# Optimization experiments

Measured on AMD Instinct MI355X. Metric: run time of the kernel, lower is better.

The kernel has to match this reference:

```python
import jax, jax.numpy as jnp
import numpy as np

EPS = 1e-5
BIG = np.int32(2 ** 30)      # sentinel larger than any voxel label
L_MAX = 1024                  # fixed upper bound on number of components (jit-friendly)


def _offsets(conn):
    # 3D neighborhood offsets with at most `conn` nonzero coordinates (skimage connectivity)
    offs = []
    for dz in (-1, 0, 1):
        for dy in (-1, 0, 1):
            for dx in (-1, 0, 1):
                nz = (dz != 0) + (dy != 0) + (dx != 0)
                if 0 < nz <= conn:
                    offs.append((dz, dy, dx))
    return offs


def _ccl_26(fg):
    """Connected-component labeling, 26-connectivity (skimage.label connectivity=3).
    Iterative min-label propagation (3x3x3 min-pool) + pointer jumping.
    Returns int32 labels: 0 = background, each component gets min(flat_index)+1."""
    shape = fg.shape
    n = fg.size
    init = jnp.where(fg, jnp.arange(1, n + 1, dtype=jnp.int32).reshape(shape), 0)

    def step(labels):
        cand = jnp.where(fg, labels, BIG)
        pooled = jax.lax.reduce_window(cand, BIG, jax.lax.min, (3, 3, 3), (1, 1, 1), 'SAME')
        new = jnp.where(fg, jnp.minimum(labels, pooled), 0)
        flat = new.ravel()
        for _ in range(2):  # pointer jumping / path compression (labels are flat_index+1)
            parent = flat[jnp.maximum(flat - 1, 0)]
            flat = jnp.where(flat > 0, parent, 0)
        return flat.reshape(shape)

    def cond(c):
        old, new = c
        return jnp.any(old != new)

    def body(c):
        _, cur = c
        return cur, step(cur)

    _, final = jax.lax.while_loop(cond, body, (init, step(init)))
    return final


def _inner_boundary_18(fg):
    """skimage find_boundaries(mode='inner', connectivity=2) on 3D binary mask:
    foreground voxel with any background voxel in its 18-neighborhood
    (fg & ~erosion(fg), reflect border handling)."""
    D, H, W = fg.shape
    p = jnp.pad(fg, 1, mode='reflect')
    eroded = fg
    for dz, dy, dx in _offsets(2):
        eroded = eroded & p[1 + dz:1 + dz + D, 1 + dy:1 + dy + H, 1 + dx:1 + dx + W]
    return fg & ~eroded


def _compactness(y_pred):
    fg = y_pred > 0.5
    labels = _ccl_26(fg)                       # [D,H,W] int32
    boundary = _inner_boundary_18(fg)          # [D,H,W] bool

    # compact per-component ids (sorted unique labels, padded with BIG to stay sorted)
    uniq = jnp.unique(labels, size=L_MAX, fill_value=BIG)
    ids = jnp.searchsorted(uniq, labels).astype(jnp.int32)

    area = jax.ops.segment_sum(fg.astype(jnp.float32).ravel(), ids.ravel(), num_segments=L_MAX)
    perim = jax.ops.segment_sum(boundary.astype(jnp.float32).ravel(), ids.ravel(), num_segments=L_MAX)

    valid = (uniq > 0) & (uniq < BIG)
    # sum over z of 4*pi*area_z / (perim_3d^2 + eps) == 4*pi*total_area / (perim^2 + eps),
    # then averaged over depth D (as in the original per-label /= shape[0]).
    per_label = jnp.where(valid, 4.0 * jnp.pi * area / (perim ** 2 + EPS), 0.0)
    return jnp.sum(per_label) / y_pred.shape[0]


def setup_inputs() -> dict:
    key = jax.random.key(0)
    y_pred = jax.random.uniform(key, (64, 256, 256), dtype=jnp.float32)
    return {"y_pred": y_pred}


def reference(y_pred) -> jnp.ndarray:
    comp = _compactness(y_pred)
    return 1.0 / (comp + EPS)
```

## Files before the change

### kernel.cpp

```cpp
#include <hip/hip_runtime.h>

#define DD 64
#define HH 256
#define WW 256
#define NN (DD*HH*WW)
#define GHS 2048
#define NCOPY 16
#define PHS 131072
#define NSEG (NN/32)

#define TZ 8
#define TY 32
#define TX 32
#define TVOX (TZ*TY*TX)

#define CA 458752
#define CB 114688
#define CFACE (CA + 4*CB)

__device__ __forceinline__ int ufind(int* P, int x){
  int p = P[x];
  while (p != x){
    int gp = P[p];
    if (gp != p) P[x] = gp;
    x = gp;
    p = P[x];
  }
  return x;
}

__device__ __forceinline__ int ufind_ro(const int* P, int x){
  int p = P[x];
  while (p != x){ x = p; p = P[x]; }
  return x;
}

__device__ __forceinline__ void uunion(int* P, int a, int b){
  while (true){
    a = ufind(P, a);
    b = ufind(P, b);
    if (a == b) return;
    if (a < b){ int t = a; a = b; b = t; }
    int old = atomicMin(&P[a], b);
    if (old == a) return;
    a = old;
  }
}

__device__ __forceinline__ int run_start(unsigned m, int x){
  unsigned zb = (~m) & ((x == 0) ? 0u : ((1u << x) - 1u));
  return (zb == 0) ? 0 : (32 - __builtin_clz(zb));
}

__device__ __forceinline__ int refl(int v, int L){ return v < 0 ? 1 : (v >= L ? L - 2 : v); }

__global__ __launch_bounds__(1024) void k_local(const float* __restrict__ in,
                                                int* __restrict__ parent,
                                                unsigned* __restrict__ fgbits,
                                                int* __restrict__ hkey,
                                                int* __restrict__ harea,
                                                int* __restrict__ hper,
                                                unsigned long long* __restrict__ ph){
  __shared__ int sl[TVOX];
  __shared__ unsigned srow[256];
  __shared__ int q[4096];
  __shared__ int qn;
  const int t = threadIdx.x;
  const int lane = t & 63;
  const int b = blockIdx.x;
  const int z0 = (b >> 6) * TZ;
  const int y0 = ((b >> 3) & 7) * TY;
  const int x0 = (b & 7) * TX;

  if (b < (NCOPY * GHS) / 1024){ int j = b * 1024 + t; hkey[j] = -1; harea[j] = 0; hper[j] = 0; }
  { int j = b * 1024 + t; if (j < PHS) ph[j] = ~0ULL; }
  if (t == 0) qn = 0;

  const int row = t >> 2;
  const int xb  = (t & 3) * 8;
  const int lz  = row >> 5, ly = row & 31;
  const int gi0 = ((z0 + lz) << 16) | ((y0 + ly) << 8) | (x0 + xb);

  float4 f0 = *(const float4*)(in + gi0);
  float4 f1 = *(const float4*)(in + gi0 + 4);
  int by = (f0.x > 0.5f)        | ((f0.y > 0.5f) << 1) |
           ((f0.z > 0.5f) << 2) | ((f0.w > 0.5f) << 3) |
           ((f1.x > 0.5f) << 4) | ((f1.y > 0.5f) << 5) |
           ((f1.z > 0.5f) << 6) | ((f1.w > 0.5f) << 7);
  int v1 = by | (__shfl_xor(by, 1) << 8);
  int v2 = v1 | (__shfl_xor(v1, 2) << 16);
  if ((t & 3) == 0){
    srow[row] = (unsigned)v2;
    fgbits[((z0 + lz) << 11) | ((y0 + ly) << 3) | (x0 >> 5)] = (unsigned)v2;
  }
  __syncthreads();

  const unsigned m = srow[row];
  const unsigned starts = m & ~(m << 1);
  const unsigned sm = starts & (0xFFu << xb);

  {
    int cnt = __popc(sm);
    int pre = cnt;
    #pragma unroll
    for (int d = 1; d < 64; d <<= 1){
      int v = __shfl_up(pre, d);
      if (lane >= d) pre += v;
    }
    int tot = __shfl(pre, 63);
    int bw = 0;
    if (lane == 63) bw = atomicAdd(&qn, tot);
    bw = __shfl(bw, 63);
    int pos = bw + pre - cnt;
    unsigned w = sm;
    while (w){
      int s = __builtin_ctz(w); w &= w - 1;
      int v = (row << 5) | s;
      sl[v] = v;
      q[pos++] = v;
    }
  }
  __syncthreads();
  const int NQ = qn;

  const int rel[4][2] = {{-1,-1},{-1,0},{-1,1},{0,-1}};
  for (int it = t; it < NQ; it += 1024){
    int v = q[it];
    int vrow = v >> 5, x = v & 31;
    unsigned mr = srow[vrow];
    unsigned zs = (~mr) >> x;
    int len = zs ? __builtin_ctz(zs) : (32 - x);
    int end = x + len - 1;
    unsigned long long wmask = ((1ull << (end + 2)) - 1) &
                               ~((x == 0) ? 0ull : ((1ull << (x - 1)) - 1));
    int vlz = vrow >> 5, vly = vrow & 31;
    #pragma unroll
    for (int r = 0; r < 4; r++){
      int zz = vlz + rel[r][0], yy = vly + rel[r][1];
      if (zz < 0 || yy < 0 || yy >= TY) continue;
      int nrow = (zz << 5) | yy;
      unsigned mN = srow[nrow];
      unsigned wm = mN & (unsigned)wmask;
      while (wm){
        int bb = __builtin_ctz(wm);
        int ns = run_start(mN, bb);
        uunion(sl, v, (nrow << 5) | ns);
        unsigned t2 = (~mN) >> bb;
        int l2 = t2 ? __builtin_ctz(t2) : (32 - bb);
        unsigned long long clr = (bb + l2 >= 32) ? 0xffffffffull : ((1ull << (bb + l2)) - 1);
        wm &= ~(unsigned)clr;
      }
    }
  }
  __syncthreads();

  for (int it = t; it < NQ; it += 1024){
    int v = q[it];
    sl[v] = ufind_ro(sl, v);
  }
  __syncthreads();

  int lab[8];
  int cur = -1;
  #pragma unroll
  for (int k = 0; k < 8; k++){
    int x = xb + k;
    if (!((m >> x) & 1)){ lab[k] = -1; cur = -1; continue; }
    if (cur < 0){
      int rs = (k == 0) ? run_start(m, x) : x;
      int r = sl[(row << 5) | rs];
      cur = ((z0 + (r >> 10)) << 16) | ((y0 + ((r >> 5) & 31)) << 8) | (x0 + (r & 31));
    }
    lab[k] = cur;
  }
  *(int4*)(parent + gi0)     = make_int4(lab[0], lab[1], lab[2], lab[3]);
  *(int4*)(parent + gi0 + 4) = make_int4(lab[4], lab[5], lab[6], lab[7]);
}

__device__ __forceinline__ void phash_union(unsigned long long* H, unsigned long long key,
                                            int* parent){
  unsigned h = (unsigned)((key * 0x9E3779B97F4A7C15ull) >> 47);
  while (true){
    unsigned long long old = atomicCAS(&H[h], ~0ULL, key);
    if (old == ~0ULL){ uunion(parent, (int)(key >> 32), (int)(key & 0xffffffffu)); return; }
    if (old == key) return;
    h = (h + 1) & (PHS - 1);
  }
}

__global__ __launch_bounds__(256) void k_pairs(int* __restrict__ parent,
                                               const unsigned* __restrict__ fgbits,
                                               unsigned long long* __restrict__ ph){
  __shared__ unsigned long long pk[256];
  const int t = threadIdx.x;
  pk[t] = ~0ULL;
  __syncthreads();

  const int nb = (int)gridDim.x;
  const int bsw = (blockIdx.x & 7) * (nb >> 3) + (blockIdx.x >> 3);
  const int id = bsw * 256 + t;
  int z, y, x, ot;
  if (id < CA){ ot = 0; z = ((id >> 16) + 1) << 3; y = (id >> 8) & 255; x = id & 255; }
  else {
    int q = id - CA;
    int f = q >> 14;
    int r = q & 16383;
    int g = f / 7, mm = f % 7;
    if      (g == 0){ ot = 1; y = (mm + 1) << 5;  z = r >> 8; x = r & 255; }
    else if (g == 1){ ot = 2; y = (mm << 5) + 31; z = r >> 8; x = r & 255; }
    else if (g == 2){ ot = 3; x = (mm + 1) << 5;  z = r >> 8; y = r & 255; }
    else            { ot = 4; x = (mm << 5) + 31; z = r >> 8; y = r & 255; }
  }
  const int s = x >> 5, xl = x & 31;
  const unsigned wself = fgbits[(z << 11) | (y << 3) | s];
  if ((wself >> xl) & 1){
    const int a = parent[(z << 16) | (y << 8) | x];
    unsigned long long lastkey = ~0ULL;

    auto do_pair = [&](int zz, int yy, int xc){
      int bl = parent[(zz << 16) | (yy << 8) | xc];
      int hi = a > bl ? a : bl, lo = a > bl ? bl : a;
      unsigned long long key = ((unsigned long long)(unsigned)hi << 32) | (unsigned)lo;
      if (key == lastkey) return;
      lastkey = key;
      unsigned h = (unsigned)((key * 0x9E3779B97F4A7C15ull) >> 56);
      for (int probe = 0; probe < 256; probe++){
        unsigned long long old = atomicCAS(&pk[h], ~0ULL, key);
        if (old == ~0ULL || old == key) return;
        h = (h + 1) & 255;
      }
      phash_union(ph, key, parent);
    };

    auto do_row = [&](int zz, int yy){
      if (zz < 0 || yy < 0 || yy >= HH) return;
      unsigned mN = fgbits[(zz << 11) | (yy << 3) | s];
      if ((mN >> xl) & 1){ do_pair(zz, yy, x); return; }
      bool l = (xl > 0) ? ((mN >> (xl - 1)) & 1)
                        : (x > 0 && ((fgbits[(zz << 11) | (yy << 3) | (s - 1)] >> 31) & 1));
      bool r = (xl < 31) ? ((mN >> (xl + 1)) & 1)
                         : (x < WW - 1 && (fgbits[(zz << 11) | (yy << 3) | (s + 1)] & 1));
      if (l) do_pair(zz, yy, x - 1);
      if (r) do_pair(zz, yy, x + 1);
    };

    auto do_bit = [&](int zz, int yy, int xc){
      if (zz < 0 || yy < 0 || yy >= HH) return;
      unsigned mN = fgbits[(zz << 11) | (yy << 3) | (xc >> 5)];
      if ((mN >> (xc & 31)) & 1) do_pair(zz, yy, xc);
    };

    switch (ot){
      case 0: do_row(z-1, y-1); do_row(z-1, y); do_row(z-1, y+1); break;
      case 1: do_row(z-1, y-1); do_row(z, y-1); break;
      case 2: do_row(z-1, y+1); break;
      case 3: do_bit(z-1, y-1, x-1); do_bit(z-1, y, x-1); do_bit(z-1, y+1, x-1);
              do_bit(z,   y-1, x-1); do_bit(z,   y, x-1); break;
      case 4: do_bit(z-1, y-1, x+1); do_bit(z-1, y, x+1); do_bit(z-1, y+1, x+1);
              do_bit(z,   y-1, x+1); break;
    }
  }
  __syncthreads();
  if (pk[t] != ~0ULL) phash_union(ph, pk[t], parent);
}

__device__ __forceinline__ void ghash_add(int* hkey, int* harea, int* hper,
                                          int key, int a, int p){
  unsigned h = ((unsigned)key * 2654435761u) >> 21;
  while (true){
    int old = atomicCAS(&hkey[h], -1, key);
    if (old == -1 || old == key){
      atomicAdd(&harea[h], a);
      if (p) atomicAdd(&hper[h], p);
      return;
    }
    h = (h + 1) & (GHS - 1);
  }
}

__global__ __launch_bounds__(1024) void k_stats(const int* __restrict__ parent,
                                                const unsigned* __restrict__ fgbits,
                                                int* __restrict__ hkey,
                                                int* __restrict__ harea,
                                                int* __restrict__ hper){
  __shared__ unsigned sfg[144];
  __shared__ unsigned sbnd[32];
  __shared__ int dk[256], da[256], dp[256];
  const int t = threadIdx.x;
  const int b = blockIdx.x;
  const int z = b >> 6;
  const int y0 = (b & 63) * 4;
  const int c = (b & (NCOPY - 1)) * GHS;

  if (t < 256){ dk[t] = -1; da[t] = 0; dp[t] = 0; }
  if (t < 144){
    int p = t / 48, q = (t / 8) % 6, s = t & 7;
    int zz = refl(z + p - 1, DD), yy = refl(y0 + q - 1, HH);
    sfg[t] = fgbits[(zz << 11) | (yy << 3) | s];
  }
  __syncthreads();

  if (t < 32){
    int ry = t >> 3, s = t & 7;
    auto W  = [&](int p, int q){ return sfg[p * 48 + q * 8 + s]; };
    auto WL = [&](int p, int q){
      unsigned w = W(p, q);
      unsigned c2 = (s > 0) ? ((sfg[p * 48 + q * 8 + s - 1] >> 31) & 1u) : ((w >> 1) & 1u);
      return (w << 1) | c2;
    };
    auto WR = [&](int p, int q){
      unsigned w = W(p, q);
      unsigned c2 = (s < 7) ? ((sfg[p * 48 + q * 8 + s + 1] & 1u) << 31) : ((w & 0x40000000u) << 1);
      return (w >> 1) | c2;
    };
    int qm = ry, qc = ry + 1, qp = ry + 2;
    unsigned own = W(1, qc);
    unsigned e = W(0, qm) & W(0, qp) & W(2, qm) & W(2, qp);
    e &= W(0, qc) & WL(0, qc) & WR(0, qc);
    e &= W(2, qc) & WL(2, qc) & WR(2, qc);
    e &= W(1, qm) & WL(1, qm) & WR(1, qm);
    e &= W(1, qp) & WL(1, qp) & WR(1, qp);
    e &= WL(1, qc) & WR(1, qc);
    sbnd[t] = own & ~e;
  }
  __syncthreads();

  const int i = b * 1024 + t;
  int lab = parent[i];
  int bnd = (lab >= 0) ? (int)((sbnd[t >> 5] >> (t & 31)) & 1) : 0;

  const int lane = t & 63;
  unsigned long long fgm = __ballot(lab >= 0);
  unsigned long long bm  = __ballot(bnd != 0);
  unsigned long long act = fgm;
  while (act){
    int leader = (int)__ffsll(act) - 1;
    int llab = __shfl(lab, leader);
    unsigned long long match = __ballot(lab == llab) & fgm;
    if (lane == leader){
      int a = (int)__popcll(match);
      int p = (int)__popcll(match & bm);
      unsigned h = ((unsigned)llab * 2654435761u) >> 24;
      bool done = false;
      for (int probe = 0; probe < 256; probe++){
        int old = atomicCAS(&dk[h], -1, llab);
        if (old == -1 || old == llab){
          atomicAdd(&da[h], a);
          if (p) atomicAdd(&dp[h], p);
          done = true; break;
        }
        h = (h + 1) & 255;
      }
      if (!done){
        int l2 = llab, pr = parent[l2];
        while (pr != l2){ l2 = pr; pr = parent[l2]; }
        ghash_add(hkey + c, harea + c, hper + c, l2, a, p);
      }
    }
    act &= ~match;
  }
  __syncthreads();
  if (t < 256 && dk[t] >= 0){
    int l2 = dk[t];
    int pr = parent[l2];
    while (pr != l2){ l2 = pr; pr = parent[l2]; }
    ghash_add(hkey + c, harea + c, hper + c, l2, da[t], dp[t]);
  }
}

__global__ __launch_bounds__(256) void k_merge(int* __restrict__ hkey,
                                               int* __restrict__ harea,
                                               int* __restrict__ hper){
  const int j = GHS + blockIdx.x * 256 + threadIdx.x;
  int key = hkey[j];
  if (key >= 0) ghash_add(hkey, harea, hper, key, harea[j], hper[j]);
}

__global__ __launch_bounds__(256) void k_fin(const int* __restrict__ hkey,
                                             const int* __restrict__ harea,
                                             const int* __restrict__ hper,
                                             float* __restrict__ out){
  __shared__ float ssum[256];
  const int t = threadIdx.x;
  float s = 0.0f;
  for (int j = t; j < GHS; j += 256){
    if (hkey[j] >= 0){
      float a = (float)harea[j];
      float p = (float)hper[j];
      s += 12.566370614359172f * a / (p * p + 1e-5f);
    }
  }
  ssum[t] = s;
  __syncthreads();
  for (int w = 128; w > 0; w >>= 1){
    if (t < w) ssum[t] += ssum[t + w];
    __syncthreads();
  }
  if (t == 0){
    float comp = ssum[0] / 64.0f;
    out[0] = 1.0f / (comp + 1e-5f);
  }
}

extern "C" void kernel_launch(void* const* d_in, const int* in_sizes, int n_in,
                              void* d_out, int out_size, void* d_ws, size_t ws_size,
                              hipStream_t stream){
  const float* y = (const float*)d_in[0];
  char* w = (char*)d_ws;
  int* parent            = (int*)w;                    w += (size_t)NN * 4;
  unsigned long long* ph = (unsigned long long*)w;     w += (size_t)PHS * 8;
  int* hkey              = (int*)w;                    w += (size_t)NCOPY * GHS * 4;
  int* harea             = (int*)w;                    w += (size_t)NCOPY * GHS * 4;
  int* hper              = (int*)w;                    w += (size_t)NCOPY * GHS * 4;
  unsigned* fgbits       = (unsigned*)w;               w += (size_t)NSEG * 4;
  float* out = (float*)d_out;

  hipLaunchKernelGGL(k_local, dim3(512),       dim3(1024), 0, stream, y, parent, fgbits, hkey, harea, hper, ph);
  hipLaunchKernelGGL(k_pairs, dim3(CFACE/256), dim3(256),  0, stream, parent, fgbits, ph);
  hipLaunchKernelGGL(k_stats, dim3(NN/1024),   dim3(1024), 0, stream, parent, fgbits, hkey, harea, hper);
  hipLaunchKernelGGL(k_merge, dim3((NCOPY-1)*GHS/256), dim3(256), 0, stream, hkey, harea, hper);
  hipLaunchKernelGGL(k_fin,   dim3(1),         dim3(256),  0, stream, hkey, harea, hper, out);
}
```

Before: 158.1 us.

## Shrink k_stats to one row per block and compute boundaries via wave shuffles

k_stats now runs 256-thread blocks that each cover a single (z,y) row, instead of 1024-thread blocks covering four rows. Each wave loads the 3x3 neighbouring bitmask words into registers and builds the 18-neighbour inner boundary with __shfl, replacing the shared-memory staging, the serial 32-thread boundary phase and a __syncthreads. This spreads the boundary work across all waves and shortens the per-block critical path. The cost is four times as many blocks, each flushing its local hash to the global tables, which adds global atomic traffic and contention on a few hot component keys.

```diff
diff --git a/kernel.cpp b/kernel.cpp
--- a/kernel.cpp
+++ b/kernel.cpp
@@ -278,58 +278,60 @@
   }
 }
 
-__global__ __launch_bounds__(1024) void k_stats(const int* __restrict__ parent,
-                                                const unsigned* __restrict__ fgbits,
-                                                int* __restrict__ hkey,
-                                                int* __restrict__ harea,
-                                                int* __restrict__ hper){
-  __shared__ unsigned sfg[144];
-  __shared__ unsigned sbnd[32];
+__global__ __launch_bounds__(256) void k_stats(const int* __restrict__ parent,
+                                               const unsigned* __restrict__ fgbits,
+                                               int* __restrict__ hkey,
+                                               int* __restrict__ harea,
+                                               int* __restrict__ hper){
   __shared__ int dk[256], da[256], dp[256];
   const int t = threadIdx.x;
   const int b = blockIdx.x;
-  const int z = b >> 6;
-  const int y0 = (b & 63) * 4;
+  const int z = b >> 8, y = b & 255;
+  const int lane = t & 63;
+  const int wv = t >> 6;
   const int c = (b & (NCOPY - 1)) * GHS;
 
-  if (t < 256){ dk[t] = -1; da[t] = 0; dp[t] = 0; }
-  if (t < 144){
-    int p = t / 48, q = (t / 8) % 6, s = t & 7;
-    int zz = refl(z + p - 1, DD), yy = refl(y0 + q - 1, HH);
-    sfg[t] = fgbits[(zz << 11) | (yy << 3) | s];
-  }
-  __syncthreads();
-
-  if (t < 32){
-    int ry = t >> 3, s = t & 7;
-    auto W  = [&](int p, int q){ return sfg[p * 48 + q * 8 + s]; };
-    auto WL = [&](int p, int q){
-      unsigned w = W(p, q);
-      unsigned c2 = (s > 0) ? ((sfg[p * 48 + q * 8 + s - 1] >> 31) & 1u) : ((w >> 1) & 1u);
-      return (w << 1) | c2;
-    };
-    auto WR = [&](int p, int q){
-      unsigned w = W(p, q);
-      unsigned c2 = (s < 7) ? ((sfg[p * 48 + q * 8 + s + 1] & 1u) << 31) : ((w & 0x40000000u) << 1);
-      return (w >> 1) | c2;
-    };
-    int qm = ry, qc = ry + 1, qp = ry + 2;
-    unsigned own = W(1, qc);
-    unsigned e = W(0, qm) & W(0, qp) & W(2, qm) & W(2, qp);
-    e &= W(0, qc) & WL(0, qc) & WR(0, qc);
-    e &= W(2, qc) & WL(2, qc) & WR(2, qc);
-    e &= W(1, qm) & WL(1, qm) & WR(1, qm);
-    e &= W(1, qp) & WL(1, qp) & WR(1, qp);
-    e &= WL(1, qc) & WR(1, qc);
-    sbnd[t] = own & ~e;
-  }
-  __syncthreads();
-
-  const int i = b * 1024 + t;
+  dk[t] = -1; da[t] = 0; dp[t] = 0;
+  __syncthreads();
+
+  unsigned wl = 0;
+  if (lane < 36){
+    int p = lane / 12, q = (lane / 4) % 3, d = lane & 3;
+    int ss = wv * 2 - 1 + d;
+    if (ss >= 0 && ss < 8){
+      int zz = refl(z + p - 1, DD), yy = refl(y + q - 1, HH);
+      wl = fgbits[(zz << 11) | (yy << 3) | ss];
+    }
+  }
+
+  const int j  = lane >> 5;
+  const int s  = wv * 2 + j;
+  const int xl = lane & 31;
+  auto SW = [&](int p, int q, int dd){ return (unsigned)__shfl((int)wl, p * 12 + q * 4 + j + 1 + dd, 64); };
+  auto W  = [&](int p, int q){ return SW(p, q, 0); };
+  auto WLf = [&](int p, int q){
+    unsigned w = W(p, q);
+    unsigned cc = (s > 0) ? ((SW(p, q, -1) >> 31) & 1u) : ((w >> 1) & 1u);
+    return (w << 1) | cc;
+  };
+  auto WRf = [&](int p, int q){
+    unsigned w = W(p, q);
+    unsigned cc = (s < 7) ? ((SW(p, q, +1) & 1u) << 31) : ((w & 0x40000000u) << 1);
+    return (w >> 1) | cc;
+  };
+  unsigned own = W(1, 1);
+  unsigned e = W(0, 0) & W(0, 2) & W(2, 0) & W(2, 2);
+  e &= W(0, 1) & WLf(0, 1) & WRf(0, 1);
+  e &= W(2, 1) & WLf(2, 1) & WRf(2, 1);
+  e &= W(1, 0) & WLf(1, 0) & WRf(1, 0);
+  e &= W(1, 2) & WLf(1, 2) & WRf(1, 2);
+  e &= WLf(1, 1) & WRf(1, 1);
+  const unsigned bndw = own & ~e;
+
+  const int i = b * 256 + t;
   int lab = parent[i];
-  int bnd = (lab >= 0) ? (int)((sbnd[t >> 5] >> (t & 31)) & 1) : 0;
-
-  const int lane = t & 63;
+  int bnd = (lab >= 0) ? (int)((bndw >> xl) & 1) : 0;
+
   unsigned long long fgm = __ballot(lab >= 0);
   unsigned long long bm  = __ballot(bnd != 0);
   unsigned long long act = fgm;
@@ -360,7 +362,7 @@
     act &= ~match;
   }
   __syncthreads();
-  if (t < 256 && dk[t] >= 0){
+  if (dk[t] >= 0){
     int l2 = dk[t];
     int pr = parent[l2];
     while (pr != l2){ l2 = pr; pr = parent[l2]; }
@@ -417,7 +419,7 @@
 
   hipLaunchKernelGGL(k_local, dim3(512),       dim3(1024), 0, stream, y, parent, fgbits, hkey, harea, hper, ph);
   hipLaunchKernelGGL(k_pairs, dim3(CFACE/256), dim3(256),  0, stream, parent, fgbits, ph);
-  hipLaunchKernelGGL(k_stats, dim3(NN/1024),   dim3(1024), 0, stream, parent, fgbits, hkey, harea, hper);
+  hipLaunchKernelGGL(k_stats, dim3(NN/256),    dim3(256),  0, stream, parent, fgbits, hkey, harea, hper);
   hipLaunchKernelGGL(k_merge, dim3((NCOPY-1)*GHS/256), dim3(256), 0, stream, hkey, harea, hper);
   hipLaunchKernelGGL(k_fin,   dim3(1),         dim3(256),  0, stream, hkey, harea, hper, out);
 }
```

Result: slower. 242.8 us (+53.6%).
